# Kernel optimization log

Measured on AMD Instinct MI355X. Metric: run time of the kernel, lower is better.

Reference implementation:

```python
import jax, jax.numpy as jnp
import numpy as np

DIM = 96
HEADS = 6
HEAD_DIM = DIM // HEADS  # 16
WIN = 8
N = WIN * WIN            # 64
C = 4 * DIM              # 384
TABLE = (2 * WIN - 1) ** 2  # 225


def setup_inputs() -> dict:
    key = jax.random.key(0)
    ks = jax.random.split(key, 12)
    B_ = 2048  # num_windows * batch = 1024 * 2
    NW = 1024
    x = jax.random.normal(ks[0], (B_, N, C), dtype=jnp.float32)
    cross_x = jax.random.normal(ks[1], (B_, N, C), dtype=jnp.float32)
    rpi = jax.random.randint(ks[2], (N, N), 0, TABLE)
    mask = jnp.zeros((NW, N, N), dtype=jnp.float32)
    s = 0.02
    Wq = jax.random.normal(ks[3], (C, DIM), dtype=jnp.float32) * s
    bq = jnp.zeros((DIM,), dtype=jnp.float32)
    Wk = jax.random.normal(ks[4], (C, DIM), dtype=jnp.float32) * s
    bk = jnp.zeros((DIM,), dtype=jnp.float32)
    Wv = jax.random.normal(ks[5], (C, C), dtype=jnp.float32) * s
    bv = jnp.zeros((C,), dtype=jnp.float32)
    Wp = jax.random.normal(ks[6], (C, C), dtype=jnp.float32) * s
    bp = jnp.zeros((C,), dtype=jnp.float32)
    rpb_table = jax.random.normal(ks[7], (TABLE, HEADS), dtype=jnp.float32) * 0.02
    return {"x": x, "cross_x": cross_x, "rpi": rpi, "mask": mask,
            "Wq": Wq, "bq": bq, "Wk": Wk, "bk": bk, "Wv": Wv, "bv": bv,
            "Wp": Wp, "bp": bp, "rpb_table": rpb_table}


def reference(x, cross_x, rpi, mask, Wq, bq, Wk, bk, Wv, bv, Wp, bp, rpb_table):
    b_, n, c = x.shape
    scale = HEAD_DIM ** (-0.5)
    # projections: q,k -> dim; v -> c (=4*dim)
    q = (x @ Wq + bq).reshape(b_, n, HEADS, HEAD_DIM).transpose(0, 2, 1, 3)
    k = (cross_x @ Wk + bk).reshape(b_, n, HEADS, HEAD_DIM).transpose(0, 2, 1, 3)
    v = (cross_x @ Wv + bv).reshape(b_, n, HEADS, c // HEADS).transpose(0, 2, 1, 3)
    attn = jnp.einsum('bhnd,bhmd->bhnm', q * scale, k)
    # relative position bias: gather (n*n,) indices -> (n, n, heads) -> (heads, n, n)
    bias = rpb_table[rpi.reshape(-1)].reshape(n, n, HEADS).transpose(2, 0, 1)
    attn = attn + bias[None]
    nw = mask.shape[0]
    attn = attn.reshape(b_ // nw, nw, HEADS, n, n) + mask[None, :, None]
    attn = attn.reshape(b_, HEADS, n, n)
    attn = jax.nn.softmax(attn, axis=-1)
    out = jnp.einsum('bhnm,bhmd->bhnd', attn, v)  # (b_, heads, n, c//heads)
    out = out.transpose(0, 2, 1, 3).reshape(b_, n, c)
    out = out @ Wp + bp
    return out
```

## Files before the change

### kernel.cpp

```cpp
#include <hip/hip_runtime.h>
#include <hip/hip_bf16.h>


typedef __attribute__((ext_vector_type(8))) short short8;
typedef __attribute__((ext_vector_type(4))) float f32x4;

__device__ __forceinline__ f32x4 mfma_b16(short8 a, short8 b, f32x4 c) {
  return __builtin_amdgcn_mfma_f32_16x16x32_bf16(a, b, c, 0, 0, 0);
}

__device__ __forceinline__ unsigned short f2bf(float x) {
  unsigned u = __builtin_bit_cast(unsigned, x);
  u = (u + 0x7fffu + ((u >> 16) & 1u)) >> 16;
  return (unsigned short)u;
}

__device__ __forceinline__ unsigned pack2(float a, float b) {
  return (unsigned)f2bf(a) | ((unsigned)f2bf(b) << 16);
}

__device__ __forceinline__ void gl_lds16(const char* g, char* l) {
  __builtin_amdgcn_global_load_lds(
      (const __attribute__((address_space(1))) unsigned int*)g,
      (__attribute__((address_space(3))) unsigned int*)l, 16, 0, 0);
}

__global__ void prep_k(const float* __restrict__ Wq, const float* __restrict__ Wk,
                       const float* __restrict__ Wv, const float* __restrict__ Wp,
                       const float* __restrict__ rpb, const int* __restrict__ rpi,
                       const float* __restrict__ bk, const float* __restrict__ bv,
                       unsigned short* __restrict__ Wq_t, unsigned short* __restrict__ Wkv_t,
                       unsigned short* __restrict__ Wp_t, float* __restrict__ bias6,
                       float* __restrict__ bias_kv) {
  const int T0 = 96 * 384, T1 = 480 * 384, T2 = 384 * 384, T3 = 6 * 4096, T4 = 480;
  int total = T0 + T1 + T2 + T3 + T4;
  for (int i = blockIdx.x * blockDim.x + threadIdx.x; i < total;
       i += gridDim.x * blockDim.x) {
    int r = i;
    if (r < T0) {
      int n = r / 384, k = r % 384;
      Wq_t[r] = f2bf(Wq[k * 96 + n]);
    } else if ((r -= T0) < T1) {
      int n = r / 384, k = r % 384;
      Wkv_t[r] = f2bf(n < 96 ? Wk[k * 96 + n] : Wv[k * 384 + (n - 96)]);
    } else if ((r -= T1) < T2) {
      int n = r / 384, k = r % 384;
      Wp_t[r] = f2bf(Wp[k * 384 + n]);
    } else if ((r -= T2) < T3) {
      int h = r >> 12, ij = r & 4095;
      bias6[r] = rpb[rpi[ij] * 6 + h];
    } else {
      r -= T3;
      bias_kv[r] = (r < 96) ? bk[r] : bv[r - 96];
    }
  }
}

template <int A_MODE, int OUT_MODE, int NX>
__global__ __launch_bounds__(256, 4) void gemm3_k(
    const void* __restrict__ Av, const unsigned short* __restrict__ Bt,
    const float* __restrict__ bias, void* __restrict__ Outv,
    unsigned short* __restrict__ k_out, unsigned short* __restrict__ vt_out) {
  __shared__ char lds[40960];
  constexpr int AB[2] = {0, 8192}, BB[2] = {16384, 28672};
  const int tid = threadIdx.x, lane = tid & 63, wid = tid >> 6;
  const int g = blockIdx.x;
  const int lg_id = (g & 7) * (NX * 256) + (g >> 3);
  const int my = lg_id / NX, nx = lg_id - my * NX;
  const int m0 = my * 64, n0 = nx * 96;
  const int wm = (wid >> 1) * 32, wn = (wid & 1) * 48;
  const int lr = lane & 15, lg = lane >> 4;

  float4 areg[4];
  const int ar = tid >> 2, aq = tid & 3;

  auto a_issue_f32 = [&](int kt) {
    const float* A = (const float*)Av + (size_t)(m0 + ar) * 384 + kt * 64 + aq * 16;
#pragma unroll
    for (int p = 0; p < 4; ++p) areg[p] = *reinterpret_cast<const float4*>(A + p * 4);
  };
  auto a_write_f32 = [&](char* Ab) {
    unsigned pk[8];
#pragma unroll
    for (int p = 0; p < 4; ++p) {
      pk[p * 2]     = pack2(areg[p].x, areg[p].y);
      pk[p * 2 + 1] = pack2(areg[p].z, areg[p].w);
    }
    const int c0 = aq * 2;
    *reinterpret_cast<uint4*>(Ab + ar * 128 + ((c0 ^ (ar & 7)) * 16)) =
        make_uint4(pk[0], pk[1], pk[2], pk[3]);
    *reinterpret_cast<uint4*>(Ab + ar * 128 + (((c0 + 1) ^ (ar & 7)) * 16)) =
        make_uint4(pk[4], pk[5], pk[6], pk[7]);
  };
  auto a_issue_lds = [&](int kt, char* Ab) {
    const char* Ag = (const char*)Av;
#pragma unroll
    for (int j = 0; j < 2; ++j) {
      const int rb = (wid * 2 + j) * 8;
      const int row = rb + (lane >> 3), c = lane & 7;
      gl_lds16(Ag + (size_t)(m0 + row) * 768 + kt * 128 + ((c ^ (row & 7)) * 16),
               Ab + rb * 128);
    }
  };
  auto b_issue = [&](int kt, char* Bb) {
#pragma unroll
    for (int j = 0; j < 3; ++j) {
      const int rb = (wid * 3 + j) * 8;
      const int row = rb + (lane >> 3), c = lane & 7;
      gl_lds16((const char*)Bt + (size_t)(n0 + row) * 768 + kt * 128 +
                   ((c ^ (row & 7)) * 16),
               Bb + rb * 128);
    }
  };

  f32x4 acc[2][3];
#pragma unroll
  for (int i = 0; i < 2; ++i)
#pragma unroll
    for (int j = 0; j < 3; ++j) acc[i][j] = (f32x4){0.f, 0.f, 0.f, 0.f};

  if (A_MODE == 0) { a_issue_f32(0); a_write_f32(lds + AB[0]); }
  else a_issue_lds(0, lds + AB[0]);
  b_issue(0, lds + BB[0]);
  __syncthreads();

  int cur = 0;
  for (int kt = 0; kt < 6; ++kt) {
    char* An = lds + AB[cur ^ 1];
    char* Bn = lds + BB[cur ^ 1];
    if (kt < 5) {
      if (A_MODE == 0) a_issue_f32(kt + 1);
      else a_issue_lds(kt + 1, An);
      b_issue(kt + 1, Bn);
    }
    {
      const char* Ab = lds + AB[cur];
      const char* Bb = lds + BB[cur];
#pragma unroll
      for (int ks = 0; ks < 2; ++ks) {
        short8 a[2], b[3];
#pragma unroll
        for (int mf = 0; mf < 2; ++mf) {
          const int row = wm + mf * 16 + lr;
          a[mf] = *reinterpret_cast<const short8*>(
              Ab + row * 128 + (((ks * 4 + lg) ^ (row & 7)) * 16));
        }
#pragma unroll
        for (int nf = 0; nf < 3; ++nf) {
          const int row = wn + nf * 16 + lr;
          b[nf] = *reinterpret_cast<const short8*>(
              Bb + row * 128 + (((ks * 4 + lg) ^ (row & 7)) * 16));
        }
#pragma unroll
        for (int mf = 0; mf < 2; ++mf)
#pragma unroll
          for (int nf = 0; nf < 3; ++nf)
            acc[mf][nf] = mfma_b16(a[mf], b[nf], acc[mf][nf]);
      }
    }
    if (kt < 5 && A_MODE == 0) a_write_f32(An);
    __syncthreads();
    cur ^= 1;
  }

  if (OUT_MODE == 0 || (OUT_MODE == 2 && nx == 0)) {
    unsigned short* dst = (OUT_MODE == 0) ? (unsigned short*)Outv : k_out;
#pragma unroll
    for (int mf = 0; mf < 2; ++mf)
#pragma unroll
      for (int nf = 0; nf < 3; ++nf) {
        const int col = wn + nf * 16 + lr;
        const float bb = bias[col];
#pragma unroll
        for (int r = 0; r < 4; ++r) {
          const int row = wm + mf * 16 + lg * 4 + r;
          *reinterpret_cast<unsigned short*>(lds + row * 208 + col * 2) =
              f2bf(acc[mf][nf][r] + bb);
        }
      }
    __syncthreads();
#pragma unroll
    for (int j = 0; j < 3; ++j) {
      const int Lb = (j * 256 + tid) * 16;
      const int row = Lb / 192, inner = Lb % 192;
      *reinterpret_cast<uint4*>((char*)dst + (size_t)(m0 + row) * 192 + inner) =
          *reinterpret_cast<const uint4*>(lds + row * 208 + inner);
    }
  } else if (OUT_MODE == 1) {
    float* outp = (float*)Outv;
#pragma unroll
    for (int mf = 0; mf < 2; ++mf)
#pragma unroll
      for (int nf = 0; nf < 3; ++nf) {
        const int col = n0 + wn + nf * 16 + lr;
        const float bb = bias[col];
#pragma unroll
        for (int r = 0; r < 4; ++r) {
          const int row = m0 + wm + mf * 16 + lg * 4 + r;
          outp[(size_t)row * 384 + col] = acc[mf][nf][r] + bb;
        }
      }
  } else {
#pragma unroll
    for (int mf = 0; mf < 2; ++mf)
#pragma unroll
      for (int nf = 0; nf < 3; ++nf) {
        const int dl = wn + nf * 16 + lr;
        const float bb = bias[n0 + dl];
        const int tok0 = wm + mf * 16 + lg * 4;
        *reinterpret_cast<unsigned*>(lds + dl * 144 + tok0 * 2) =
            pack2(acc[mf][nf][0] + bb, acc[mf][nf][1] + bb);
        *reinterpret_cast<unsigned*>(lds + dl * 144 + tok0 * 2 + 4) =
            pack2(acc[mf][nf][2] + bb, acc[mf][nf][3] + bb);
      }
    __syncthreads();
#pragma unroll
    for (int j = 0; j < 3; ++j) {
      const int Lc = j * 256 + tid;
      const int dl = Lc >> 3, c = Lc & 7;
      *reinterpret_cast<uint4*>((char*)vt_out + (size_t)my * 49152 +
                                (size_t)((nx - 1) * 96 + dl) * 128 + c * 16) =
          *reinterpret_cast<const uint4*>(lds + dl * 144 + c * 16);
    }
  }
}

__global__ __launch_bounds__(256) void attn_k(
    const unsigned short* __restrict__ q_buf, const unsigned short* __restrict__ k_buf,
    const unsigned short* __restrict__ vt_buf, const float* __restrict__ bias6,
    const float* __restrict__ mask, unsigned short* __restrict__ att_out) {
  __shared__ unsigned short vt_lds[384 * 64];
  __shared__ float S[64 * 68];
  __shared__ unsigned short P[64 * 64];
  const int w = blockIdx.x;
  const int tid = threadIdx.x;
  const int lane = tid & 63, wid = tid >> 6;

  const unsigned short* vsrc = vt_buf + (size_t)w * 24576;
#pragma unroll
  for (int p = 0; p < 12; ++p) {
    int e = (p * 256 + tid) * 8;
    int d = e >> 6, j = e & 63;
    const float4 v = *reinterpret_cast<const float4*>(vsrc + e);
    *reinterpret_cast<float4*>((char*)vt_lds + ((d * 128 + j * 2) ^ ((d & 7) << 4))) = v;
  }
  __syncthreads();

  const float* maskw = mask + (size_t)(w & 1023) * 4096;
  const int ti = wid;
  const int lr = lane & 15, lg = lane >> 4;
  const int srow = tid >> 2, sq = tid & 3;

  for (int h = 0; h < 6; ++h) {
    short8 afrag = {0, 0, 0, 0, 0, 0, 0, 0};
    if (lg < 2)
      afrag = *reinterpret_cast<const short8*>(
          q_buf + (size_t)(w * 64 + ti * 16 + lr) * 96 + h * 16 + lg * 8);
#pragma unroll
    for (int tj = 0; tj < 4; ++tj) {
      short8 bfrag = {0, 0, 0, 0, 0, 0, 0, 0};
      if (lg < 2)
        bfrag = *reinterpret_cast<const short8*>(
            k_buf + (size_t)(w * 64 + tj * 16 + lr) * 96 + h * 16 + lg * 8);
      f32x4 zero = {0.f, 0.f, 0.f, 0.f};
      f32x4 s = mfma_b16(afrag, bfrag, zero);
#pragma unroll
      for (int r = 0; r < 4; ++r) {
        int i = ti * 16 + lg * 4 + r;
        int j = tj * 16 + lr;
        S[i * 68 + j] = s[r] * 0.25f + bias6[h * 4096 + i * 64 + j] + maskw[i * 64 + j];
      }
    }
    float buf[16];
    float mx = -3.0e38f;
#pragma unroll
    for (int c = 0; c < 16; ++c) {
      buf[c] = S[srow * 68 + sq * 16 + c];
      mx = fmaxf(mx, buf[c]);
    }
    mx = fmaxf(mx, __shfl_xor(mx, 1));
    mx = fmaxf(mx, __shfl_xor(mx, 2));
    float sum = 0.f;
#pragma unroll
    for (int c = 0; c < 16; ++c) {
      buf[c] = __expf(buf[c] - mx);
      sum += buf[c];
    }
    sum += __shfl_xor(sum, 1);
    sum += __shfl_xor(sum, 2);
    float inv = 1.0f / sum;
#pragma unroll
    for (int c = 0; c < 16; c += 2) {
      unsigned pk = pack2(buf[c] * inv, buf[c + 1] * inv);
      *reinterpret_cast<unsigned*>(
          (char*)P + ((srow * 128 + (sq * 16 + c) * 2) ^ ((srow & 7) << 4))) = pk;
    }
    short8 pa[2];
#pragma unroll
    for (int ks = 0; ks < 2; ++ks) {
      int i = ti * 16 + lr;
      pa[ks] = *reinterpret_cast<const short8*>(
          (char*)P + ((i * 128 + ks * 64 + lg * 16) ^ ((i & 7) << 4)));
    }
#pragma unroll
    for (int td = 0; td < 4; ++td) {
      f32x4 o = {0.f, 0.f, 0.f, 0.f};
#pragma unroll
      for (int ks = 0; ks < 2; ++ks) {
        int dd = h * 64 + td * 16 + lr;
        short8 vb = *reinterpret_cast<const short8*>(
            (char*)vt_lds + ((dd * 128 + ks * 64 + lg * 16) ^ ((dd & 7) << 4)));
        o = mfma_b16(pa[ks], vb, o);
      }
#pragma unroll
      for (int r = 0; r < 4; ++r) {
        int token = w * 64 + ti * 16 + lg * 4 + r;
        int col = h * 64 + td * 16 + lr;
        att_out[(size_t)token * 384 + col] = f2bf(o[r]);
      }
    }
  }
}

extern "C" void kernel_launch(void* const* d_in, const int* in_sizes, int n_in,
                              void* d_out, int out_size, void* d_ws, size_t ws_size,
                              hipStream_t stream) {
  const float* x    = (const float*)d_in[0];
  const float* cx   = (const float*)d_in[1];
  const int*   rpi  = (const int*)d_in[2];
  const float* mask = (const float*)d_in[3];
  const float* Wq   = (const float*)d_in[4];
  const float* bq   = (const float*)d_in[5];
  const float* Wk   = (const float*)d_in[6];
  const float* bk   = (const float*)d_in[7];
  const float* Wv   = (const float*)d_in[8];
  const float* bv   = (const float*)d_in[9];
  const float* Wp   = (const float*)d_in[10];
  const float* bp   = (const float*)d_in[11];
  const float* rpb  = (const float*)d_in[12];

  char* ws = (char*)d_ws;
  unsigned short* Wq_t   = (unsigned short*)(ws + 0);
  unsigned short* Wkv_t  = (unsigned short*)(ws + 73728);
  unsigned short* Wp_t   = (unsigned short*)(ws + 442368);
  float*          bias6  = (float*)(ws + 737280);
  float*          biaskv = (float*)(ws + 835584);
  const size_t MB = 1u << 20;
  unsigned short* q_buf  = (unsigned short*)(ws + MB);
  unsigned short* k_buf  = (unsigned short*)(ws + MB + 25165824u);
  unsigned short* vt_buf = (unsigned short*)(ws + MB + 50331648u);
  unsigned short* att    = (unsigned short*)(ws + MB + 150994944u);

  prep_k<<<256, 256, 0, stream>>>(Wq, Wk, Wv, Wp, rpb, rpi, bk, bv,
                                  Wq_t, Wkv_t, Wp_t, bias6, biaskv);
  gemm3_k<0, 0, 1><<<2048, 256, 0, stream>>>(x, Wq_t, bq, q_buf, nullptr, nullptr);
  gemm3_k<0, 2, 5><<<10240, 256, 0, stream>>>(cx, Wkv_t, biaskv, nullptr, k_buf, vt_buf);
  attn_k<<<2048, 256, 0, stream>>>(q_buf, k_buf, vt_buf, bias6, mask, att);
  gemm3_k<1, 1, 4><<<8192, 256, 0, stream>>>(att, Wp_t, bp, d_out, nullptr, nullptr);
}
```

Measured before the change: 401.5 us.

## Fuse attention with output projection GEMM in one per-window kernel

Merges the attention kernel and the final projection GEMM into a single kernel: each block computes softmax attention for one window, keeps the 64x384 bf16 result in LDS, then multiplies it by Wp streamed through double-buffered LDS tiles. The aim is to drop the round trip of the intermediate attention tensor through global memory and one kernel launch. It also computes scores transposed so softmax runs in registers without an fp32 S buffer, pre-swizzles the V^T layout at write time for direct global-to-LDS copies, and uses the library bf16 conversion. In exchange it needs large LDS (80KB) and a register stash, which may limit occupancy.

```diff
diff --git a/kernel.cpp b/kernel.cpp
--- a/kernel.cpp
+++ b/kernel.cpp
@@ -10,13 +10,15 @@
 }
 
 __device__ __forceinline__ unsigned short f2bf(float x) {
-  unsigned u = __builtin_bit_cast(unsigned, x);
-  u = (u + 0x7fffu + ((u >> 16) & 1u)) >> 16;
-  return (unsigned short)u;
+  return __builtin_bit_cast(unsigned short, __float2bfloat16(x));
 }
 
 __device__ __forceinline__ unsigned pack2(float a, float b) {
   return (unsigned)f2bf(a) | ((unsigned)f2bf(b) << 16);
+}
+
+__device__ __forceinline__ int swz48(int c, int r) {
+  return (c & ~7) | ((c ^ r) & 7);
 }
 
 __device__ __forceinline__ void gl_lds16(const char* g, char* l) {
@@ -92,16 +94,6 @@
     *reinterpret_cast<uint4*>(Ab + ar * 128 + (((c0 + 1) ^ (ar & 7)) * 16)) =
         make_uint4(pk[4], pk[5], pk[6], pk[7]);
   };
-  auto a_issue_lds = [&](int kt, char* Ab) {
-    const char* Ag = (const char*)Av;
-#pragma unroll
-    for (int j = 0; j < 2; ++j) {
-      const int rb = (wid * 2 + j) * 8;
-      const int row = rb + (lane >> 3), c = lane & 7;
-      gl_lds16(Ag + (size_t)(m0 + row) * 768 + kt * 128 + ((c ^ (row & 7)) * 16),
-               Ab + rb * 128);
-    }
-  };
   auto b_issue = [&](int kt, char* Bb) {
 #pragma unroll
     for (int j = 0; j < 3; ++j) {
@@ -119,8 +111,8 @@
 #pragma unroll
     for (int j = 0; j < 3; ++j) acc[i][j] = (f32x4){0.f, 0.f, 0.f, 0.f};
 
-  if (A_MODE == 0) { a_issue_f32(0); a_write_f32(lds + AB[0]); }
-  else a_issue_lds(0, lds + AB[0]);
+  a_issue_f32(0);
+  a_write_f32(lds + AB[0]);
   b_issue(0, lds + BB[0]);
   __syncthreads();
 
@@ -129,8 +121,7 @@
     char* An = lds + AB[cur ^ 1];
     char* Bn = lds + BB[cur ^ 1];
     if (kt < 5) {
-      if (A_MODE == 0) a_issue_f32(kt + 1);
-      else a_issue_lds(kt + 1, An);
+      a_issue_f32(kt + 1);
       b_issue(kt + 1, Bn);
     }
     {
@@ -158,7 +149,7 @@
             acc[mf][nf] = mfma_b16(a[mf], b[nf], acc[mf][nf]);
       }
     }
-    if (kt < 5 && A_MODE == 0) a_write_f32(An);
+    if (kt < 5) a_write_f32(An);
     __syncthreads();
     cur ^= 1;
   }
@@ -186,20 +177,6 @@
       *reinterpret_cast<uint4*>((char*)dst + (size_t)(m0 + row) * 192 + inner) =
           *reinterpret_cast<const uint4*>(lds + row * 208 + inner);
     }
-  } else if (OUT_MODE == 1) {
-    float* outp = (float*)Outv;
-#pragma unroll
-    for (int mf = 0; mf < 2; ++mf)
-#pragma unroll
-      for (int nf = 0; nf < 3; ++nf) {
-        const int col = n0 + wn + nf * 16 + lr;
-        const float bb = bias[col];
-#pragma unroll
-        for (int r = 0; r < 4; ++r) {
-          const int row = m0 + wm + mf * 16 + lg * 4 + r;
-          outp[(size_t)row * 384 + col] = acc[mf][nf][r] + bb;
-        }
-      }
   } else {
 #pragma unroll
     for (int mf = 0; mf < 2; ++mf)
@@ -219,106 +196,181 @@
       const int Lc = j * 256 + tid;
       const int dl = Lc >> 3, c = Lc & 7;
       *reinterpret_cast<uint4*>((char*)vt_out + (size_t)my * 49152 +
-                                (size_t)((nx - 1) * 96 + dl) * 128 + c * 16) =
+                                (size_t)((nx - 1) * 96 + dl) * 128 +
+                                ((c ^ (dl & 7)) << 4)) =
           *reinterpret_cast<const uint4*>(lds + dl * 144 + c * 16);
     }
   }
 }
 
-__global__ __launch_bounds__(256) void attn_k(
+__global__ __launch_bounds__(256, 2) void ap_k(
     const unsigned short* __restrict__ q_buf, const unsigned short* __restrict__ k_buf,
     const unsigned short* __restrict__ vt_buf, const float* __restrict__ bias6,
-    const float* __restrict__ mask, unsigned short* __restrict__ att_out) {
-  __shared__ unsigned short vt_lds[384 * 64];
-  __shared__ float S[64 * 68];
-  __shared__ unsigned short P[64 * 64];
+    const float* __restrict__ mask, const unsigned short* __restrict__ Wp_t,
+    const float* __restrict__ bp, float* __restrict__ out) {
+  __shared__ char lds[81920];
+  const int tid = threadIdx.x, lane = tid & 63, wid = tid >> 6;
+  const int lr = lane & 15, lg = lane >> 4;
   const int w = blockIdx.x;
-  const int tid = threadIdx.x;
-  const int lane = tid & 63, wid = tid >> 6;
-
-  const unsigned short* vsrc = vt_buf + (size_t)w * 24576;
-#pragma unroll
-  for (int p = 0; p < 12; ++p) {
-    int e = (p * 256 + tid) * 8;
-    int d = e >> 6, j = e & 63;
-    const float4 v = *reinterpret_cast<const float4*>(vsrc + e);
-    *reinterpret_cast<float4*>((char*)vt_lds + ((d * 128 + j * 2) ^ ((d & 7) << 4))) = v;
-  }
+
+  auto b_issue = [&](int T, char* Bb) {
+    const int nc = T / 6, kt = T - nc * 6;
+#pragma unroll
+    for (int j = 0; j < 3; ++j) {
+      const int rb = (wid * 3 + j) * 8;
+      const int row = rb + (lane >> 3), c = lane & 7;
+      gl_lds16((const char*)Wp_t + (size_t)(nc * 96 + row) * 768 + kt * 128 +
+                   ((c ^ (row & 7)) * 16),
+               Bb + rb * 128);
+    }
+  };
+
+  const char* vsrc = (const char*)vt_buf + (size_t)w * 49152;
+#pragma unroll
+  for (int j = 0; j < 12; ++j) {
+    const int off = (wid * 12 + j) * 1024;
+    gl_lds16(vsrc + off + lane * 16, lds + off);
+  }
+  b_issue(0, lds + 57344);
+  b_issue(1, lds + 57344 + 12288);
   __syncthreads();
 
-  const float* maskw = mask + (size_t)(w & 1023) * 4096;
-  const int ti = wid;
-  const int lr = lane & 15, lg = lane >> 4;
-  const int srow = tid >> 2, sq = tid & 3;
+  unsigned stash[48];
+  char* Plds = lds + 49152;
+  const float* mw = mask + (size_t)(w & 1023) * 4096;
+  const int iq = wid * 16 + lr;
 
   for (int h = 0; h < 6; ++h) {
-    short8 afrag = {0, 0, 0, 0, 0, 0, 0, 0};
+    short8 qa = {0, 0, 0, 0, 0, 0, 0, 0};
     if (lg < 2)
-      afrag = *reinterpret_cast<const short8*>(
-          q_buf + (size_t)(w * 64 + ti * 16 + lr) * 96 + h * 16 + lg * 8);
+      qa = *reinterpret_cast<const short8*>(
+          q_buf + (size_t)(w * 64 + iq) * 96 + h * 16 + lg * 8);
+    float sv[4][4];
 #pragma unroll
     for (int tj = 0; tj < 4; ++tj) {
-      short8 bfrag = {0, 0, 0, 0, 0, 0, 0, 0};
+      short8 kf = {0, 0, 0, 0, 0, 0, 0, 0};
       if (lg < 2)
-        bfrag = *reinterpret_cast<const short8*>(
+        kf = *reinterpret_cast<const short8*>(
             k_buf + (size_t)(w * 64 + tj * 16 + lr) * 96 + h * 16 + lg * 8);
-      f32x4 zero = {0.f, 0.f, 0.f, 0.f};
-      f32x4 s = mfma_b16(afrag, bfrag, zero);
+      f32x4 z = {0.f, 0.f, 0.f, 0.f};
+      f32x4 s = mfma_b16(kf, qa, z);
+      const int j0 = tj * 16 + lg * 4;
+      const float4 bi = *reinterpret_cast<const float4*>(bias6 + h * 4096 + iq * 64 + j0);
+      const float4 mk = *reinterpret_cast<const float4*>(mw + iq * 64 + j0);
+      sv[tj][0] = s[0] * 0.25f + bi.x + mk.x;
+      sv[tj][1] = s[1] * 0.25f + bi.y + mk.y;
+      sv[tj][2] = s[2] * 0.25f + bi.z + mk.z;
+      sv[tj][3] = s[3] * 0.25f + bi.w + mk.w;
+    }
+    float mx = sv[0][0];
+#pragma unroll
+    for (int tj = 0; tj < 4; ++tj)
+#pragma unroll
+      for (int r = 0; r < 4; ++r) mx = fmaxf(mx, sv[tj][r]);
+    mx = fmaxf(mx, __shfl_xor(mx, 16));
+    mx = fmaxf(mx, __shfl_xor(mx, 32));
+    float sum = 0.f;
+#pragma unroll
+    for (int tj = 0; tj < 4; ++tj)
 #pragma unroll
       for (int r = 0; r < 4; ++r) {
-        int i = ti * 16 + lg * 4 + r;
-        int j = tj * 16 + lr;
-        S[i * 68 + j] = s[r] * 0.25f + bias6[h * 4096 + i * 64 + j] + maskw[i * 64 + j];
-      }
-    }
-    float buf[16];
-    float mx = -3.0e38f;
-#pragma unroll
-    for (int c = 0; c < 16; ++c) {
-      buf[c] = S[srow * 68 + sq * 16 + c];
-      mx = fmaxf(mx, buf[c]);
-    }
-    mx = fmaxf(mx, __shfl_xor(mx, 1));
-    mx = fmaxf(mx, __shfl_xor(mx, 2));
-    float sum = 0.f;
-#pragma unroll
-    for (int c = 0; c < 16; ++c) {
-      buf[c] = __expf(buf[c] - mx);
-      sum += buf[c];
-    }
-    sum += __shfl_xor(sum, 1);
-    sum += __shfl_xor(sum, 2);
-    float inv = 1.0f / sum;
-#pragma unroll
-    for (int c = 0; c < 16; c += 2) {
-      unsigned pk = pack2(buf[c] * inv, buf[c + 1] * inv);
-      *reinterpret_cast<unsigned*>(
-          (char*)P + ((srow * 128 + (sq * 16 + c) * 2) ^ ((srow & 7) << 4))) = pk;
+        sv[tj][r] = __expf(sv[tj][r] - mx);
+        sum += sv[tj][r];
+      }
+    sum += __shfl_xor(sum, 16);
+    sum += __shfl_xor(sum, 32);
+    const float inv = 1.0f / sum;
+#pragma unroll
+    for (int tj = 0; tj < 4; ++tj) {
+      const int c = tj * 2 + (lg >> 1);
+      uint2 st;
+      st.x = pack2(sv[tj][0] * inv, sv[tj][1] * inv);
+      st.y = pack2(sv[tj][2] * inv, sv[tj][3] * inv);
+      *reinterpret_cast<uint2*>(Plds + iq * 128 + ((c ^ (iq & 7)) << 4) +
+                                (lg & 1) * 8) = st;
     }
     short8 pa[2];
 #pragma unroll
-    for (int ks = 0; ks < 2; ++ks) {
-      int i = ti * 16 + lr;
+    for (int ks = 0; ks < 2; ++ks)
       pa[ks] = *reinterpret_cast<const short8*>(
-          (char*)P + ((i * 128 + ks * 64 + lg * 16) ^ ((i & 7) << 4)));
-    }
+          Plds + iq * 128 + (((ks * 4 + lg) ^ (iq & 7)) << 4));
 #pragma unroll
     for (int td = 0; td < 4; ++td) {
       f32x4 o = {0.f, 0.f, 0.f, 0.f};
 #pragma unroll
       for (int ks = 0; ks < 2; ++ks) {
-        int dd = h * 64 + td * 16 + lr;
+        const int d = h * 64 + td * 16 + lr;
         short8 vb = *reinterpret_cast<const short8*>(
-            (char*)vt_lds + ((dd * 128 + ks * 64 + lg * 16) ^ ((dd & 7) << 4)));
-        o = mfma_b16(pa[ks], vb, o);
-      }
-#pragma unroll
-      for (int r = 0; r < 4; ++r) {
-        int token = w * 64 + ti * 16 + lg * 4 + r;
-        int col = h * 64 + td * 16 + lr;
-        att_out[(size_t)token * 384 + col] = f2bf(o[r]);
-      }
-    }
+            lds + d * 128 + (((ks * 4 + lg) ^ (d & 7)) << 4));
+        o = mfma_b16(vb, pa[ks], o);
+      }
+      stash[h * 8 + td * 2 + 0] = pack2(o[0], o[1]);
+      stash[h * 8 + td * 2 + 1] = pack2(o[2], o[3]);
+    }
+  }
+  __syncthreads();
+
+#pragma unroll
+  for (int h = 0; h < 6; ++h)
+#pragma unroll
+    for (int td = 0; td < 4; ++td)
+#pragma unroll
+      for (int p2 = 0; p2 < 2; ++p2) {
+        const int c0 = h * 64 + td * 16 + lg * 4 + p2 * 2;
+        *reinterpret_cast<unsigned*>(
+            lds + iq * 768 + swz48(c0 >> 3, iq) * 16 + ((c0 * 2) & 15)) =
+            stash[h * 8 + td * 2 + p2];
+      }
+  __syncthreads();
+
+  const int wm = (wid >> 1) * 32, wn = (wid & 1) * 48;
+  f32x4 acc[2][3];
+#pragma unroll
+  for (int i = 0; i < 2; ++i)
+#pragma unroll
+    for (int j = 0; j < 3; ++j) acc[i][j] = (f32x4){0.f, 0.f, 0.f, 0.f};
+
+  for (int T = 0; T < 24; ++T) {
+    const int nc = T / 6, kt = T - nc * 6;
+    if (T >= 1 && T < 23) b_issue(T + 1, lds + 57344 + ((T + 1) & 1) * 12288);
+    const char* Bb = lds + 57344 + (T & 1) * 12288;
+#pragma unroll
+    for (int ks = 0; ks < 2; ++ks) {
+      short8 a[2], b[3];
+#pragma unroll
+      for (int mf = 0; mf < 2; ++mf) {
+        const int row = wm + mf * 16 + lr;
+        a[mf] = *reinterpret_cast<const short8*>(
+            lds + row * 768 + swz48(kt * 8 + ks * 4 + lg, row) * 16);
+      }
+#pragma unroll
+      for (int nf = 0; nf < 3; ++nf) {
+        const int row = wn + nf * 16 + lr;
+        b[nf] = *reinterpret_cast<const short8*>(
+            Bb + row * 128 + (((ks * 4 + lg) ^ (row & 7)) * 16));
+      }
+#pragma unroll
+      for (int mf = 0; mf < 2; ++mf)
+#pragma unroll
+        for (int nf = 0; nf < 3; ++nf)
+          acc[mf][nf] = mfma_b16(a[mf], b[nf], acc[mf][nf]);
+    }
+    if (kt == 5) {
+#pragma unroll
+      for (int mf = 0; mf < 2; ++mf)
+#pragma unroll
+        for (int nf = 0; nf < 3; ++nf) {
+          const int col = nc * 96 + wn + nf * 16 + lr;
+          const float bb = bp[col];
+#pragma unroll
+          for (int r = 0; r < 4; ++r) {
+            const int row = wm + mf * 16 + lg * 4 + r;
+            out[(size_t)(w * 64 + row) * 384 + col] = acc[mf][nf][r] + bb;
+          }
+          acc[mf][nf] = (f32x4){0.f, 0.f, 0.f, 0.f};
+        }
+    }
+    __syncthreads();
   }
 }
 
@@ -349,12 +401,11 @@
   unsigned short* q_buf  = (unsigned short*)(ws + MB);
   unsigned short* k_buf  = (unsigned short*)(ws + MB + 25165824u);
   unsigned short* vt_buf = (unsigned short*)(ws + MB + 50331648u);
-  unsigned short* att    = (unsigned short*)(ws + MB + 150994944u);
 
   prep_k<<<256, 256, 0, stream>>>(Wq, Wk, Wv, Wp, rpb, rpi, bk, bv,
                                   Wq_t, Wkv_t, Wp_t, bias6, biaskv);
   gemm3_k<0, 0, 1><<<2048, 256, 0, stream>>>(x, Wq_t, bq, q_buf, nullptr, nullptr);
   gemm3_k<0, 2, 5><<<10240, 256, 0, stream>>>(cx, Wkv_t, biaskv, nullptr, k_buf, vt_buf);
-  attn_k<<<2048, 256, 0, stream>>>(q_buf, k_buf, vt_buf, bias6, mask, att);
-  gemm3_k<1, 1, 4><<<8192, 256, 0, stream>>>(att, Wp_t, bp, d_out, nullptr, nullptr);
-}
+  ap_k<<<2048, 256, 0, stream>>>(q_buf, k_buf, vt_buf, bias6, mask, Wp_t, bp,
+                                 (float*)d_out);
+}
```

Result: faster. 347.9 us, median of 3 (-13.4%).
